# Performance work log

Hardware: AMD Instinct MI355X
Metric: run time of the kernel (lower is better)

The kernel has to match this reference:

```python
import jax, jax.numpy as jnp
import numpy as np

EPS = 1e-5

def _ln(x, g, b):
    mu = jnp.mean(x, axis=-1, keepdims=True)
    var = jnp.mean((x - mu) ** 2, axis=-1, keepdims=True)
    return (x - mu) / jnp.sqrt(var + EPS) * g + b

def _aft(x, q_w, q_b, k_w, k_b, v_w, v_b, p_w, p_b, wbias):
    # AFTFull: Yt = sigmoid(Q) * (exp(wbias) @ (exp(K)*V)) / (exp(wbias) @ exp(K))
    T = x.shape[1]
    Q = x @ q_w + q_b
    K = x @ k_w + k_b
    V = x @ v_w + v_b
    ew = jnp.exp(wbias[:T, :T])                      # [T, T]
    eK = jnp.exp(K)                                   # [B, T, H]
    num = jnp.einsum('ts,bsh->bth', ew, eK * V)
    den = jnp.einsum('ts,bsh->bth', ew, eK)
    Yt = jax.nn.sigmoid(Q) * (num / den)
    return Yt @ p_w + p_b

def setup_inputs() -> dict:
    key = jax.random.key(0)
    B, T, D, H = 8, 2048, 256, 256
    MAXT = 2048
    std = 1.0 / np.sqrt(H)
    names_shapes = [
        ('fc_w', (D, H)), ('fc_b', (H,)),
        ('q_w', (H, H)), ('q_b', (H,)),
        ('k_w', (H, H)), ('k_b', (H,)),
        ('v_w', (H, H)), ('v_b', (H,)),
        ('p_w', (H, H)), ('p_b', (H,)),
        ('wbias', (MAXT, MAXT)),
        ('n1_g', (H,)), ('n1_b', (H,)),
        ('n2_g', (H,)), ('n2_b', (H,)),
        ('w_i', (H, H)), ('u_i', (H, H)), ('b_i', (H,)),
        ('w_f', (H, H)), ('u_f', (H, H)), ('b_f', (H,)),
        ('w_c', (H, H)), ('u_c', (H, H)), ('b_c', (H,)),
        ('w_o', (H, H)), ('u_o', (H, H)), ('b_o', (H,)),
    ]
    keys = jax.random.split(key, len(names_shapes) + 1)
    inp = {'x': jax.random.normal(keys[0], (B, T, D), dtype=jnp.float32)}
    for k, (name, shp) in zip(keys[1:], names_shapes):
        inp[name] = jax.random.uniform(k, shp, dtype=jnp.float32, minval=-std, maxval=std)
    return inp

def reference(x, fc_w, fc_b, q_w, q_b, k_w, k_b, v_w, v_b, p_w, p_b, wbias,
              n1_g, n1_b, n2_g, n2_b,
              w_i, u_i, b_i, w_f, u_f, b_f, w_c, u_c, b_c, w_o, u_o, b_o):
    xf = x @ fc_w + fc_b                              # [B, T, H]
    att = _aft(xf, q_w, q_b, k_w, k_b, v_w, v_b, p_w, p_b, wbias)
    # original calls self.norm(x_) but discards the result -> only relu applies
    filt = jax.nn.relu(att)
    afx = _ln(att, n1_g, n1_b)
    prod = _ln(filt * afx, n2_g, n2_b)                # [B, T, H]
    B, T, H = prod.shape
    h0 = jnp.zeros((B, H), prod.dtype)
    c0 = jnp.zeros((B, H), prod.dtype)
    def step(carry, x_t):
        h, c = carry
        i = jax.nn.sigmoid(x_t @ w_i + h @ u_i + b_i)
        f = jax.nn.sigmoid(x_t @ w_f + h @ u_f + b_f)
        g = jnp.tanh(x_t @ w_c + h @ u_c + b_c)
        o = jax.nn.sigmoid(x_t @ w_o + h @ u_o + b_o)
        c = f * c + i * g
        h = o * jnp.tanh(c)
        return (h, c), h
    (h_t, c_t), hs = jax.lax.scan(step, (h0, c0), prod.transpose(1, 0, 2))
    hidden_seq = hs.transpose(1, 0, 2)                # [B, T, H]
    return hidden_seq, h_t, c_t
```

## Files before the change

### kernel.cpp

```cpp
#include <hip/hip_runtime.h>


typedef unsigned short u16;
typedef unsigned int   u32;
typedef u16 u16x4 __attribute__((ext_vector_type(4)));
typedef u16 u16x8 __attribute__((ext_vector_type(8)));
typedef u32 u32x4 __attribute__((ext_vector_type(4)));
typedef short s16x8 __attribute__((ext_vector_type(8)));
typedef float f32x4 __attribute__((ext_vector_type(4)));
typedef _Float16 f16x2 __attribute__((ext_vector_type(2)));

typedef __attribute__((address_space(3))) void* lds_vp;
typedef const __attribute__((address_space(1))) void* gbl_vp;
#define GLDS(gp, lp) __builtin_amdgcn_global_load_lds((gbl_vp)(gp), (lds_vp)(lp), 16, 0, 0)

__device__ __forceinline__ float b2f(u16 u){
  union { u32 i; float f; } c; c.i = ((u32)u) << 16; return c.f;
}
__device__ __forceinline__ u16 f2b(float f){
  union { float f; u32 i; } c; c.f = f;
  u32 i = c.i;
  return (u16)((i + 0x7FFFu + ((i >> 16) & 1u)) >> 16);
}
__device__ __forceinline__ u16 f2h_bits(float f){
  _Float16 h = (_Float16)f;
  return __builtin_bit_cast(u16, h);
}
__device__ __forceinline__ float dot2(u32 a, u32 b, float acc){
#if __has_builtin(__builtin_amdgcn_fdot2)
  return __builtin_amdgcn_fdot2(__builtin_bit_cast(f16x2, a),
                                __builtin_bit_cast(f16x2, b), acc, false);
#else
  f16x2 x = __builtin_bit_cast(f16x2, a), y = __builtin_bit_cast(f16x2, b);
  return acc + (float)x[0]*(float)y[0] + (float)x[1]*(float)y[1];
#endif
}
__device__ __forceinline__ float sigm(float x){ return 1.f/(1.f + __expf(-x)); }
__device__ __forceinline__ float tanh_f(float x){
  float e = __expf(-2.f * fmaxf(x, -44.f));
  return (1.f - e)/(1.f + e);
}

__global__ void k_detect(const u16* __restrict__ x, int* __restrict__ flag){
  const int l = threadIdx.x;
  const u16 u = x[l];
  const float v = b2f(u);
  const int bad = !(v == v) || fabsf(v) > 1e4f || (v != 0.f && fabsf(v) < 1e-30f);
  const int zev = ((l & 1) == 0) && (u == 0);
  unsigned long long mb = __ballot(bad);
  unsigned long long mz = __ballot(zev);
  if (l == 0) *flag = (mb != 0ull || __popcll(mz) >= 24) ? 1 : 0;
}

__global__ __launch_bounds__(256) void k_cvt_x(const void* __restrict__ xin,
    u16* __restrict__ xb, const int* __restrict__ flag){
  const int isf = *flag;
  const size_t e = ((size_t)blockIdx.x*256 + threadIdx.x)*8;
  u16x8 o;
  if (isf){
    const float* p = (const float*)xin + e;
    f32x4 a = *(const f32x4*)p, b = *(const f32x4*)(p+4);
    o[0]=f2b(a[0]);o[1]=f2b(a[1]);o[2]=f2b(a[2]);o[3]=f2b(a[3]);
    o[4]=f2b(b[0]);o[5]=f2b(b[1]);o[6]=f2b(b[2]);o[7]=f2b(b[3]);
  } else {
    o = *(const u16x8*)((const u16*)xin + e);
  }
  *(u16x8*)(xb + e) = o;
}

template<int EPI>
__global__ __launch_bounds__(256)
void k_gemm(const u16* __restrict__ A, const u16* __restrict__ Bt,
            void* __restrict__ C, const u16* __restrict__ bias,
            const u16* __restrict__ aux,
            int M, int N, int K, int lda, int ldb, int ldc,
            long bsB , long bsC )
{
  __shared__ __align__(16) u16 As[128*32];
  __shared__ __align__(16) u16 Bs[128*32];
  const int tid = threadIdx.x;
  const int wv = tid >> 6, l = tid & 63;
  const int m0 = blockIdx.x * 128, n0 = blockIdx.y * 128;
  const u16* Bp = Bt + (size_t)blockIdx.z * bsB;
  char* Cp = (char*)C + (size_t)blockIdx.z * bsC;

  const int rL = wv*16 + (l >> 2);
  const int cL = (l & 3) * 8;
  const u16* gA = A  + (size_t)(m0 + rL)*lda + cL;
  const u16* gB = Bp + (size_t)(n0 + rL)*ldb + cL;
  u16* lA = As + wv*512 + l*8;
  u16* lB = Bs + wv*512 + l*8;

  f32x4 acc[4][4];
  #pragma unroll
  for (int m=0;m<4;++m)
    #pragma unroll
    for (int n=0;n<4;++n) acc[m][n] = f32x4{0.f,0.f,0.f,0.f};

  const int wr = wv >> 1, wc = wv & 1;
  const int lr = l & 15, lk = (l >> 4) * 8, lq = l >> 4;
  const int nk = K >> 5;
  for (int kt = 0; kt < nk; ++kt){
    __syncthreads();
    GLDS(gA,                  lA);
    GLDS(gA + (size_t)64*lda, lA + 2048);
    GLDS(gB,                  lB);
    GLDS(gB + (size_t)64*ldb, lB + 2048);
    gA += 32; gB += 32;
    __syncthreads();
    s16x8 af[4], bfr[4];
    #pragma unroll
    for (int m=0;m<4;++m) af[m]  = *(const s16x8*)&As[(wr*64 + m*16 + lr)*32 + lk];
    #pragma unroll
    for (int n=0;n<4;++n) bfr[n] = *(const s16x8*)&Bs[(wc*64 + n*16 + lr)*32 + lk];
    #pragma unroll
    for (int m=0;m<4;++m)
      #pragma unroll
      for (int n=0;n<4;++n)
        acc[m][n] = __builtin_amdgcn_mfma_f32_16x16x32_bf16(af[m], bfr[n], acc[m][n], 0, 0, 0);
  }

  #pragma unroll
  for (int m=0;m<4;++m){
    const int gr0 = m0 + wr*64 + m*16 + lq*4;
    #pragma unroll
    for (int n=0;n<4;++n){
      const int gc = n0 + wc*64 + n*16 + lr;
      f32x4 v = acc[m][n];
      if constexpr (EPI == 0 || EPI == 1){
        const float bb = b2f(bias[gc]);
        u16* Cb = (u16*)Cp;
        #pragma unroll
        for (int r=0;r<4;++r){
          float xv = v[r] + bb;
          if constexpr (EPI == 1) xv = sigm(xv);
          Cb[(size_t)(gr0 + r)*ldc + gc] = f2b(xv);
        }
      } else if constexpr (EPI == 2){
        u16* Cb = (u16*)Cp;
        #pragma unroll
        for (int r=0;r<4;++r) Cb[(size_t)(gr0 + r)*ldc + gc] = f2b(v[r]);
      } else {
        const float bb = b2f(bias[gc]);
        u16x4 ekv, ek;
        #pragma unroll
        for (int r=0;r<4;++r){
          float e  = __expf(v[r] + bb);
          float vv = b2f(aux[(size_t)(gr0 + r)*256 + gc]);
          ek[r]  = f2b(e);
          ekv[r] = f2b(e * vv);
        }
        const int z = gr0 >> 11, t0 = gr0 & 2047;
        u16* base = (u16*)Cp + ((size_t)z*512 + gc)*2048 + t0;
        *(u16x4*)base = ekv;
        *(u16x4*)(base + (size_t)256*2048) = ek;
      }
    }
  }
}

struct TJobs { const void* src[13]; u16* dst[13]; int mode[13]; };

__global__ __launch_bounds__(256) void k_transpose(TJobs jb, const int* __restrict__ flag){
  const int isf = *flag;
  const int mz = blockIdx.y;
  const void* in = jb.src[mz]; u16* out = jb.dst[mz]; const int mode = jb.mode[mz];
  const int bi = blockIdx.x >> 2, bj = blockIdx.x & 3;
  __shared__ float tile[64][65];
  const int tid = threadIdx.x;
  const int r = tid >> 3, c = (tid & 7) * 8;
  #pragma unroll
  for (int it=0; it<2; ++it){
    const size_t base = (size_t)(bi*64 + it*32 + r)*256 + bj*64 + c;
    float vals[8];
    if (isf){
      const float* p = (const float*)in + base;
      f32x4 a = *(const f32x4*)p, b = *(const f32x4*)(p+4);
      vals[0]=a[0];vals[1]=a[1];vals[2]=a[2];vals[3]=a[3];
      vals[4]=b[0];vals[5]=b[1];vals[6]=b[2];vals[7]=b[3];
    } else {
      u16x8 v = *(const u16x8*)((const u16*)in + base);
      #pragma unroll
      for (int u=0;u<8;++u) vals[u] = b2f(v[u]);
    }
    #pragma unroll
    for (int u=0;u<8;++u) tile[it*32 + r][c+u] = vals[u];
  }
  __syncthreads();
  #pragma unroll
  for (int it=0; it<2; ++it){
    const int rr = it*32 + r;
    u16x8 o;
    #pragma unroll
    for (int u=0;u<8;++u){
      float xv = tile[c+u][rr];
      o[u] = mode ? f2h_bits(xv) : f2b(xv);
    }
    *(u16x8*)(out + (size_t)(bj*64 + rr)*256 + bi*64 + c) = o;
  }
}

struct PJobs { const void* src[13]; };

__global__ __launch_bounds__(256) void k_pack_params(PJobs pj, u16* __restrict__ pp,
                                                     const int* __restrict__ flag){
  const int isf = *flag;
  const int t = threadIdx.x, bid = blockIdx.x;
  const void* s = pj.src[bid];
  const float v = isf ? ((const float*)s)[t] : b2f(((const u16*)s)[t]);
  pp[bid*256 + t] = f2b(v);
}

__global__ __launch_bounds__(256) void k_expw(const void* __restrict__ wb,
    u16* __restrict__ ew, const int* __restrict__ flag){
  const int isf = *flag;
  const size_t e = ((size_t)blockIdx.x*256 + threadIdx.x)*8;
  u16x8 o;
  if (isf){
    const float* p = (const float*)wb + e;
    f32x4 a = *(const f32x4*)p, b = *(const f32x4*)(p+4);
    o[0]=f2b(__expf(a[0]));o[1]=f2b(__expf(a[1]));o[2]=f2b(__expf(a[2]));o[3]=f2b(__expf(a[3]));
    o[4]=f2b(__expf(b[0]));o[5]=f2b(__expf(b[1]));o[6]=f2b(__expf(b[2]));o[7]=f2b(__expf(b[3]));
  } else {
    u16x8 v = *(const u16x8*)((const u16*)wb + e);
    #pragma unroll
    for (int u=0;u<8;++u) o[u] = f2b(__expf(b2f(v[u])));
  }
  *(u16x8*)(ew + e) = o;
}

__global__ __launch_bounds__(256) void k_yt(const u16* __restrict__ sQ,
                                            const u16* __restrict__ nd,
                                            u16* __restrict__ yt){
  const int e = blockIdx.x*256 + threadIdx.x;
  const int m = e >> 6, n = (e & 63) << 2;
  const size_t ndb = ((size_t)(m >> 11)*2048 + (size_t)(m & 2047))*512 + n;
  u16x4 num = *(const u16x4*)(nd + ndb);
  u16x4 den = *(const u16x4*)(nd + ndb + 256);
  u16x4 q4  = *(const u16x4*)(sQ + (size_t)m*256 + n);
  u16x4 o;
  #pragma unroll
  for (int u=0;u<4;++u) o[u] = f2b(b2f(q4[u]) * b2f(num[u]) / b2f(den[u]));
  *(u16x4*)(yt + (size_t)m*256 + n) = o;
}

__device__ __forceinline__ float bsum(float v, float* red){
  #pragma unroll
  for (int o=1;o<64;o<<=1) v += __shfl_xor(v, o, 64);
  __syncthreads();
  if ((threadIdx.x & 63) == 0) red[threadIdx.x >> 6] = v;
  __syncthreads();
  return red[0]+red[1]+red[2]+red[3];
}

__global__ __launch_bounds__(256) void k_lnprod(const u16* __restrict__ att,
    const u16* __restrict__ pp, u16* __restrict__ prod){
  __shared__ float red[4];
  const int row = blockIdx.x, j = threadIdx.x;
  const u16* g1 = pp + 1280; const u16* b1 = pp + 1536;
  const u16* g2 = pp + 1792; const u16* b2_ = pp + 2048;
  const float a = b2f(att[(size_t)row*256 + j]);
  const float mu  = bsum(a, red) * (1.f/256.f);
  const float d   = a - mu;
  const float var = bsum(d*d, red) * (1.f/256.f);
  const float afx = d * rsqrtf(var + 1e-5f) * b2f(g1[j]) + b2f(b1[j]);
  const float y   = fmaxf(a, 0.f) * afx;
  const float mu2  = bsum(y, red) * (1.f/256.f);
  const float d2   = y - mu2;
  const float var2 = bsum(d2*d2, red) * (1.f/256.f);
  const float o = d2 * rsqrtf(var2 + 1e-5f) * b2f(g2[j]) + b2f(b2_[j]);
  prod[(size_t)row*256 + j] = f2b(o);
}

__global__ __launch_bounds__(1024)
void k_lstm3(const u16* __restrict__ P, const u16* __restrict__ UT,
             void* __restrict__ outv, const int* __restrict__ flag)
{
  const int isf = *flag;
  const int b = blockIdx.x;
  const int tid = threadIdx.x;
  const int g = tid >> 8, col = tid & 255;

  __shared__ u32x4 Wl4[8][1024];
  __shared__ __align__(16) u16 hl16[2][256];
  __shared__ float pre[1024];

  const u32x4* wq = (const u32x4*)((const u32*)UT + (size_t)tid*128);
  u32x4 wr[24];
  #pragma unroll
  for (int j=0;j<24;++j) wr[j] = wq[j];
  #pragma unroll
  for (int j=0;j<8;++j) Wl4[j][tid] = wq[24+j];
  #pragma unroll
  for (int j=0;j<24;++j)
    asm volatile("" : "+v"(wr[j].x), "+v"(wr[j].y), "+v"(wr[j].z), "+v"(wr[j].w));

  if (tid < 256){ hl16[0][tid] = 0; hl16[1][tid] = 0; }
  float c_state = 0.f, h_cur = 0.f;
  const u16* Pb = P + (size_t)b*2048*1024;
  u16 pn = Pb[tid];
  __syncthreads();

  int cur = 0;
  for (int t=0; t<2048; ++t){
    const float pcur = b2f(pn);
    if (t < 2047) pn = Pb[(size_t)(t+1)*1024 + tid];

    const u32x4* hb = (const u32x4*)&hl16[cur][0];
    float s0 = 0.f, s1 = 0.f;
    #pragma unroll
    for (int j=0;j<24;++j){
      const u32x4 h4 = hb[j];
      s0 = dot2(h4.x, wr[j].x, s0);
      s1 = dot2(h4.y, wr[j].y, s1);
      s0 = dot2(h4.z, wr[j].z, s0);
      s1 = dot2(h4.w, wr[j].w, s1);
    }
    #pragma unroll
    for (int j=0;j<8;++j){
      const u32x4 h4 = hb[24+j];
      const u32x4 wt = Wl4[j][tid];
      s0 = dot2(h4.x, wt.x, s0);
      s1 = dot2(h4.y, wt.y, s1);
      s0 = dot2(h4.z, wt.z, s0);
      s1 = dot2(h4.w, wt.w, s1);
    }
    pre[tid] = s0 + s1 + pcur;
    __syncthreads();

    if (g == 0){
      const float gi_ = sigm(pre[col]);
      const float gf_ = sigm(pre[256 + col]);
      const float gg_ = tanh_f(pre[512 + col]);
      const float go_ = sigm(pre[768 + col]);
      c_state = gf_*c_state + gi_*gg_;
      h_cur = go_ * tanh_f(c_state);
      hl16[cur ^ 1][col] = f2h_bits(h_cur);
      const size_t oe = (size_t)b*524288 + (size_t)t*256 + col;
      if (isf) ((float*)outv)[oe] = h_cur;
      else     ((u16*)outv)[oe]   = f2b(h_cur);
    }
    __syncthreads();
    cur ^= 1;
  }

  if (g == 0){
    const size_t o1 = 4194304 + (size_t)b*256 + col;
    if (isf){ ((float*)outv)[o1] = h_cur; ((float*)outv)[o1 + 2048] = c_state; }
    else    { ((u16*)outv)[o1] = f2b(h_cur); ((u16*)outv)[o1 + 2048] = f2b(c_state); }
  }
}

extern "C" void kernel_launch(void* const* d_in, const int* in_sizes, int n_in,
                              void* d_out, int out_size, void* d_ws, size_t ws_size,
                              hipStream_t stream)
{
  const void* x    = d_in[0];
  const void* fc_w = d_in[1];  const void* fc_b = d_in[2];
  const void* q_w  = d_in[3];  const void* q_b  = d_in[4];
  const void* k_w  = d_in[5];  const void* k_b  = d_in[6];
  const void* v_w  = d_in[7];  const void* v_b  = d_in[8];
  const void* p_w  = d_in[9];  const void* p_b  = d_in[10];
  const void* wbias= d_in[11];
  const void* n1g  = d_in[12]; const void* n1b  = d_in[13];
  const void* n2g  = d_in[14]; const void* n2b  = d_in[15];
  const void* w_i  = d_in[16]; const void* u_i  = d_in[17];
  const void* b_i  = d_in[18];
  const void* w_f  = d_in[19]; const void* u_f  = d_in[20];
  const void* b_f  = d_in[21];
  const void* w_c  = d_in[22]; const void* u_c  = d_in[23];
  const void* b_c  = d_in[24];
  const void* w_o  = d_in[25]; const void* u_o  = d_in[26];
  const void* b_o  = d_in[27];

  char* w = (char*)d_ws;
  u16* ew   = (u16*)(w + 0);
  u16* WT   = (u16*)(w + 8388608);
  u16* UT   = (u16*)(w + 9568256);
  u16* pp   = (u16*)(w + 10092544);
  int* flag = (int*)(w + 10099200);
  u16* xf   = (u16*)(w + 10099712);
  u16* Vb   = (u16*)(w + 18488320);
  u16* sQ   = (u16*)(w + 26876928);
  u16* ekvT = (u16*)(w + 35265536);
  u16* nd   = (u16*)(w + 52042752);
  u16* xb   = ekvT;
  u16* yt   = xf;
  u16* att  = Vb;
  u16* prod = sQ;
  u16* P    = ekvT;

  k_detect<<<1, 64, 0, stream>>>((const u16*)x, flag);

  k_cvt_x<<<2048, 256, 0, stream>>>(x, xb, flag);
  TJobs jb;
  const void* srcs[13] = {fc_w, q_w, k_w, v_w, p_w, w_i, w_f, w_c, w_o, u_i, u_f, u_c, u_o};
  for (int i=0;i<13;++i){
    jb.src[i]  = srcs[i];
    jb.dst[i]  = (i < 9) ? (WT + (size_t)i*65536) : (UT + (size_t)(i-9)*65536);
    jb.mode[i] = (i < 9) ? 0 : 1;
  }
  k_transpose<<<dim3(16,13), 256, 0, stream>>>(jb, flag);
  PJobs pj;
  const void* psrc[13] = {fc_b, q_b, k_b, v_b, p_b, n1g, n1b, n2g, n2b, b_i, b_f, b_c, b_o};
  for (int i=0;i<13;++i) pj.src[i] = psrc[i];
  k_pack_params<<<13, 256, 0, stream>>>(pj, pp, flag);

  k_expw<<<2048, 256, 0, stream>>>(wbias, ew, flag);

  k_gemm<0><<<dim3(128,2,1), 256, 0, stream>>>(xb, WT + 0*65536, xf, pp + 0, nullptr,
      16384,256,256, 256,256,256, 0,0);
  k_gemm<0><<<dim3(128,2,1), 256, 0, stream>>>(xf, WT + 3*65536, Vb, pp + 768, nullptr,
      16384,256,256, 256,256,256, 0,0);
  k_gemm<1><<<dim3(128,2,1), 256, 0, stream>>>(xf, WT + 1*65536, sQ, pp + 256, nullptr,
      16384,256,256, 256,256,256, 0,0);
  k_gemm<3><<<dim3(128,2,1), 256, 0, stream>>>(xf, WT + 2*65536, ekvT, pp + 512, Vb,
      16384,256,256, 256,256,2048, 0,0);

  k_gemm<2><<<dim3(16,4,8), 256, 0, stream>>>(ew, ekvT, nd, nullptr, nullptr,
      2048,512,2048, 2048,2048,512, (long)512*2048, (long)2048*512*2);

  k_yt<<<4096, 256, 0, stream>>>(sQ, nd, yt);

  k_gemm<0><<<dim3(128,2,1), 256, 0, stream>>>(yt, WT + 4*65536, att, pp + 1024, nullptr,
      16384,256,256, 256,256,256, 0,0);

  k_lnprod<<<16384, 256, 0, stream>>>(att, pp, prod);

  k_gemm<0><<<dim3(128,8,1), 256, 0, stream>>>(prod, WT + 5*65536, P, pp + 2304, nullptr,
      16384,1024,256, 256,256,1024, 0,0);

  k_lstm3<<<8, 1024, 0, stream>>>(P, UT, d_out, flag);
}
```

Baseline: 3.539 ms.

## Split LSTM recurrence over k-quarters with shuffle reduction, one barrier per step

The LSTM kernel now gives each group of 4 threads one hidden unit. Each thread computes partial dot products over a quarter of h for all four gates and combines them with xor shuffles. This removes the shared pre-activation buffer and one of the two __syncthreads per timestep. The input-projection GEMM epilogue writes gate columns interleaved per hidden unit, so one u16x4 load fetches all four gate inputs, and h is stored in a padded LDS layout to avoid bank conflicts. Only 1 in 4 threads runs the nonlinearities, and the weight indexing into UT is restructured, so it relies on the existing UT layout matching.

```diff
diff --git a/kernel.cpp b/kernel.cpp
--- a/kernel.cpp
+++ b/kernel.cpp
@@ -127,14 +127,15 @@
     for (int n=0;n<4;++n){
       const int gc = n0 + wc*64 + n*16 + lr;
       f32x4 v = acc[m][n];
-      if constexpr (EPI == 0 || EPI == 1){
+      if constexpr (EPI == 0 || EPI == 1 || EPI == 4){
         const float bb = b2f(bias[gc]);
         u16* Cb = (u16*)Cp;
+        const int cc = (EPI == 4) ? (((gc & 255) << 2) + (gc >> 8)) : gc;
         #pragma unroll
         for (int r=0;r<4;++r){
           float xv = v[r] + bb;
           if constexpr (EPI == 1) xv = sigm(xv);
-          Cb[(size_t)(gr0 + r)*ldc + gc] = f2b(xv);
+          Cb[(size_t)(gr0 + r)*ldc + cc] = f2b(xv);
         }
       } else if constexpr (EPI == 2){
         u16* Cb = (u16*)Cp;
@@ -273,79 +274,74 @@
 }
 
 __global__ __launch_bounds__(1024)
-void k_lstm3(const u16* __restrict__ P, const u16* __restrict__ UT,
+void k_lstm4(const u16* __restrict__ P4, const u16* __restrict__ UT,
              void* __restrict__ outv, const int* __restrict__ flag)
 {
   const int isf = *flag;
   const int b = blockIdx.x;
   const int tid = threadIdx.x;
-  const int g = tid >> 8, col = tid & 255;
+  const int cq = tid >> 2, s = tid & 3;
 
   __shared__ u32x4 Wl4[8][1024];
-  __shared__ __align__(16) u16 hl16[2][256];
-  __shared__ float pre[1024];
-
-  const u32x4* wq = (const u32x4*)((const u32*)UT + (size_t)tid*128);
-  u32x4 wr[24];
-  #pragma unroll
-  for (int j=0;j<24;++j) wr[j] = wq[j];
-  #pragma unroll
-  for (int j=0;j<8;++j) Wl4[j][tid] = wq[24+j];
-  #pragma unroll
-  for (int j=0;j<24;++j)
-    asm volatile("" : "+v"(wr[j].x), "+v"(wr[j].y), "+v"(wr[j].z), "+v"(wr[j].w));
-
-  if (tid < 256){ hl16[0][tid] = 0; hl16[1][tid] = 0; }
+  __shared__ __align__(16) u16 hl16[2][288];
+
+  const u32* Ub = (const u32*)UT + (size_t)cq*128 + (size_t)s*32;
+  u32x4 wv[24];
+  #pragma unroll
+  for (int j=0;j<8;++j){
+    wv[j]       = *(const u32x4*)(Ub + 0*32768 + j*4);
+    wv[8+j]     = *(const u32x4*)(Ub + 1*32768 + j*4);
+    wv[16+j]    = *(const u32x4*)(Ub + 2*32768 + j*4);
+    Wl4[j][tid] = *(const u32x4*)(Ub + 3*32768 + j*4);
+  }
+
+  if (tid < 288) hl16[0][tid] = 0;
   float c_state = 0.f, h_cur = 0.f;
-  const u16* Pb = P + (size_t)b*2048*1024;
-  u16 pn = Pb[tid];
+  const u16* Pb = P4 + (size_t)b*2048*1024;
+  u16x4 pn{0,0,0,0};
+  if (s == 0) pn = *(const u16x4*)(Pb + (size_t)cq*4);
   __syncthreads();
 
-  int cur = 0;
   for (int t=0; t<2048; ++t){
-    const float pcur = b2f(pn);
-    if (t < 2047) pn = Pb[(size_t)(t+1)*1024 + tid];
-
-    const u32x4* hb = (const u32x4*)&hl16[cur][0];
-    float s0 = 0.f, s1 = 0.f;
-    #pragma unroll
-    for (int j=0;j<24;++j){
-      const u32x4 h4 = hb[j];
-      s0 = dot2(h4.x, wr[j].x, s0);
-      s1 = dot2(h4.y, wr[j].y, s1);
-      s0 = dot2(h4.z, wr[j].z, s0);
-      s1 = dot2(h4.w, wr[j].w, s1);
+    const u16* hq = &hl16[t & 1][s*72];
+    float s0=0.f, s1=0.f, s2=0.f, s3=0.f;
+    #pragma unroll
+    for (int j=0;j<8;++j){
+      const u32x4 h4 = *(const u32x4*)(hq + j*8);
+      const u32x4 w3 = Wl4[j][tid];
+      s0 = dot2(h4.x, wv[j].x, s0);    s0 = dot2(h4.y, wv[j].y, s0);
+      s0 = dot2(h4.z, wv[j].z, s0);    s0 = dot2(h4.w, wv[j].w, s0);
+      s1 = dot2(h4.x, wv[8+j].x, s1);  s1 = dot2(h4.y, wv[8+j].y, s1);
+      s1 = dot2(h4.z, wv[8+j].z, s1);  s1 = dot2(h4.w, wv[8+j].w, s1);
+      s2 = dot2(h4.x, wv[16+j].x, s2); s2 = dot2(h4.y, wv[16+j].y, s2);
+      s2 = dot2(h4.z, wv[16+j].z, s2); s2 = dot2(h4.w, wv[16+j].w, s2);
+      s3 = dot2(h4.x, w3.x, s3);       s3 = dot2(h4.y, w3.y, s3);
+      s3 = dot2(h4.z, w3.z, s3);       s3 = dot2(h4.w, w3.w, s3);
     }
-    #pragma unroll
-    for (int j=0;j<8;++j){
-      const u32x4 h4 = hb[24+j];
-      const u32x4 wt = Wl4[j][tid];
-      s0 = dot2(h4.x, wt.x, s0);
-      s1 = dot2(h4.y, wt.y, s1);
-      s0 = dot2(h4.z, wt.z, s0);
-      s1 = dot2(h4.w, wt.w, s1);
-    }
-    pre[tid] = s0 + s1 + pcur;
-    __syncthreads();
-
-    if (g == 0){
-      const float gi_ = sigm(pre[col]);
-      const float gf_ = sigm(pre[256 + col]);
-      const float gg_ = tanh_f(pre[512 + col]);
-      const float go_ = sigm(pre[768 + col]);
+    s0 += __shfl_xor(s0, 1, 64); s0 += __shfl_xor(s0, 2, 64);
+    s1 += __shfl_xor(s1, 1, 64); s1 += __shfl_xor(s1, 2, 64);
+    s2 += __shfl_xor(s2, 1, 64); s2 += __shfl_xor(s2, 2, 64);
+    s3 += __shfl_xor(s3, 1, 64); s3 += __shfl_xor(s3, 2, 64);
+
+    if (s == 0){
+      const float gi_ = sigm(s0 + b2f(pn[0]));
+      const float gf_ = sigm(s1 + b2f(pn[1]));
+      const float gg_ = tanh_f(s2 + b2f(pn[2]));
+      const float go_ = sigm(s3 + b2f(pn[3]));
       c_state = gf_*c_state + gi_*gg_;
       h_cur = go_ * tanh_f(c_state);
-      hl16[cur ^ 1][col] = f2h_bits(h_cur);
-      const size_t oe = (size_t)b*524288 + (size_t)t*256 + col;
+      hl16[(t + 1) & 1][(cq >> 6)*72 + (cq & 63)] = f2h_bits(h_cur);
+      const size_t oe = (size_t)b*524288 + (size_t)t*256 + cq;
       if (isf) ((float*)outv)[oe] = h_cur;
       else     ((u16*)outv)[oe]   = f2b(h_cur);
+      if (t < 2047)
+        pn = *(const u16x4*)(Pb + (size_t)(t+1)*1024 + (size_t)cq*4);
     }
     __syncthreads();
-    cur ^= 1;
-  }
-
-  if (g == 0){
-    const size_t o1 = 4194304 + (size_t)b*256 + col;
+  }
+
+  if (s == 0){
+    const size_t o1 = 4194304 + (size_t)b*256 + cq;
     if (isf){ ((float*)outv)[o1] = h_cur; ((float*)outv)[o1 + 2048] = c_state; }
     else    { ((u16*)outv)[o1] = f2b(h_cur); ((u16*)outv)[o1 + 2048] = f2b(c_state); }
   }
@@ -427,8 +423,8 @@
 
   k_lnprod<<<16384, 256, 0, stream>>>(att, pp, prod);
 
-  k_gemm<0><<<dim3(128,8,1), 256, 0, stream>>>(prod, WT + 5*65536, P, pp + 2304, nullptr,
+  k_gemm<4><<<dim3(128,8,1), 256, 0, stream>>>(prod, WT + 5*65536, P, pp + 2304, nullptr,
       16384,1024,256, 256,256,1024, 0,0);
 
-  k_lstm3<<<8, 1024, 0, stream>>>(P, UT, d_out, flag);
-}
+  k_lstm4<<<8, 1024, 0, stream>>>(P, UT, d_out, flag);
+}
```

Result: slower. 4.887 ms (+38.1%).

## Interleave LSTM gates across lanes and exchange via shuffles, dropping one barrier

Applied to the files above, without the earlier changes.

The input-projection GEMM now writes its output with gate-interleaved columns (col*4+gate). This lets each group of four adjacent LSTM threads hold the i/f/g/o pre-activations for one hidden unit. The four gate values are exchanged with xor-shuffles instead of a shared-memory buffer, which removes one __syncthreads per timestep from the serial 2048-step loop. In exchange, all four lanes redundantly compute the gate nonlinearities, and the recurrent-weight rows are loaded with a permuted index.

```diff
diff --git a/kernel.cpp b/kernel.cpp
--- a/kernel.cpp
+++ b/kernel.cpp
@@ -127,14 +127,15 @@
     for (int n=0;n<4;++n){
       const int gc = n0 + wc*64 + n*16 + lr;
       f32x4 v = acc[m][n];
-      if constexpr (EPI == 0 || EPI == 1){
+      if constexpr (EPI == 0 || EPI == 1 || EPI == 4){
         const float bb = b2f(bias[gc]);
         u16* Cb = (u16*)Cp;
+        const int cc = (EPI == 4) ? (((gc & 255) << 2) + (gc >> 8)) : gc;
         #pragma unroll
         for (int r=0;r<4;++r){
           float xv = v[r] + bb;
           if constexpr (EPI == 1) xv = sigm(xv);
-          Cb[(size_t)(gr0 + r)*ldc + gc] = f2b(xv);
+          Cb[(size_t)(gr0 + r)*ldc + cc] = f2b(xv);
         }
       } else if constexpr (EPI == 2){
         u16* Cb = (u16*)Cp;
@@ -273,19 +274,19 @@
 }
 
 __global__ __launch_bounds__(1024)
-void k_lstm3(const u16* __restrict__ P, const u16* __restrict__ UT,
+void k_lstm7(const u16* __restrict__ P4, const u16* __restrict__ UT,
              void* __restrict__ outv, const int* __restrict__ flag)
 {
   const int isf = *flag;
   const int b = blockIdx.x;
   const int tid = threadIdx.x;
-  const int g = tid >> 8, col = tid & 255;
+  const int g = tid & 3, col = tid >> 2;
+  const int gc = g*256 + col;
 
   __shared__ u32x4 Wl4[8][1024];
   __shared__ __align__(16) u16 hl16[2][256];
-  __shared__ float pre[1024];
-
-  const u32x4* wq = (const u32x4*)((const u32*)UT + (size_t)tid*128);
+
+  const u32x4* wq = (const u32x4*)((const u32*)UT + (size_t)gc*128);
   u32x4 wr[24];
   #pragma unroll
   for (int j=0;j<24;++j) wr[j] = wq[j];
@@ -297,7 +298,7 @@
 
   if (tid < 256){ hl16[0][tid] = 0; hl16[1][tid] = 0; }
   float c_state = 0.f, h_cur = 0.f;
-  const u16* Pb = P + (size_t)b*2048*1024;
+  const u16* Pb = P4 + (size_t)b*2048*1024;
   u16 pn = Pb[tid];
   __syncthreads();
 
@@ -325,23 +326,32 @@
       s0 = dot2(h4.z, wt.z, s0);
       s1 = dot2(h4.w, wt.w, s1);
     }
-    pre[tid] = s0 + s1 + pcur;
-    __syncthreads();
-
+    const float sp = s0 + s1 + pcur;
+
+    const float a  = __shfl_xor(sp, 1, 64);
+    const float bq = __shfl_xor(sp, 2, 64);
+    const float cq = __shfl_xor(a,  2, 64);
+    const float p0 = (g==0)? sp : (g==1)? a : (g==2)? bq : cq;
+    const float p1 = (g==1)? sp : (g==0)? a : (g==3)? bq : cq;
+    const float p2 = (g==2)? sp : (g==3)? a : (g==0)? bq : cq;
+    const float p3 = (g==3)? sp : (g==2)? a : (g==1)? bq : cq;
+
+    const float gi_ = sigm(p0);
+    const float gf_ = sigm(p1);
+    const float gg_ = tanh_f(p2);
+    const float go_ = sigm(p3);
+    c_state = gf_*c_state + gi_*gg_;
+    h_cur = go_ * tanh_f(c_state);
+
+    const int nxt = cur ^ 1;
     if (g == 0){
-      const float gi_ = sigm(pre[col]);
-      const float gf_ = sigm(pre[256 + col]);
-      const float gg_ = tanh_f(pre[512 + col]);
-      const float go_ = sigm(pre[768 + col]);
-      c_state = gf_*c_state + gi_*gg_;
-      h_cur = go_ * tanh_f(c_state);
-      hl16[cur ^ 1][col] = f2h_bits(h_cur);
+      hl16[nxt][col] = f2h_bits(h_cur);
       const size_t oe = (size_t)b*524288 + (size_t)t*256 + col;
       if (isf) ((float*)outv)[oe] = h_cur;
       else     ((u16*)outv)[oe]   = f2b(h_cur);
     }
     __syncthreads();
-    cur ^= 1;
+    cur = nxt;
   }
 
   if (g == 0){
@@ -427,8 +437,8 @@
 
   k_lnprod<<<16384, 256, 0, stream>>>(att, pp, prod);
 
-  k_gemm<0><<<dim3(128,8,1), 256, 0, stream>>>(prod, WT + 5*65536, P, pp + 2304, nullptr,
+  k_gemm<4><<<dim3(128,8,1), 256, 0, stream>>>(prod, WT + 5*65536, P, pp + 2304, nullptr,
       16384,1024,256, 256,256,1024, 0,0);
 
-  k_lstm3<<<8, 1024, 0, stream>>>(P, UT, d_out, flag);
-}
+  k_lstm7<<<8, 1024, 0, stream>>>(P, UT, d_out, flag);
+}
```

New measurement: 4.655 ms. 31.5% more time.
